# Performance work log

Measured on AMD Instinct MI355X. Metric: run time of the kernel, lower is better.

The kernel has to match this reference:

```python
import jax, jax.numpy as jnp
import numpy as np

WS = (7, 7, 7)
SS = (3, 3, 3)
SEQ = WS[0] * WS[1] * WS[2]  # 343
EPS = 1e-5


def layer_norm(x, w, b):
    mu = jnp.mean(x, axis=-1, keepdims=True)
    var = jnp.mean((x - mu) ** 2, axis=-1, keepdims=True)
    return (x - mu) * jax.lax.rsqrt(var + EPS) * w + b


def window_partition(x, ws):
    b, d, h, w, c = x.shape
    x = x.reshape(b, d // ws[0], ws[0], h // ws[1], ws[1], w // ws[2], ws[2], c)
    return x.transpose(0, 1, 3, 5, 2, 4, 6, 7).reshape(-1, ws[0] * ws[1] * ws[2], c)


def window_reverse(win, ws, dims):
    b, dp, hp, wp = dims
    x = win.reshape(b, dp // ws[0], hp // ws[1], wp // ws[2], ws[0], ws[1], ws[2], -1)
    return x.transpose(0, 1, 4, 2, 5, 3, 6, 7).reshape(b, dp, hp, wp, -1)


def _rel_pos_index():
    coords = np.stack(np.meshgrid(np.arange(WS[0]), np.arange(WS[1]), np.arange(WS[2]), indexing='ij'))
    cf = coords.reshape(3, -1)
    rel = (cf[:, :, None] - cf[:, None, :]).transpose(1, 2, 0)  # (s, s, 3)
    rel[..., 0] += WS[0] - 1
    rel[..., 1] += WS[1] - 1
    rel[..., 2] += WS[2] - 1
    idx = rel[..., 0] * (2 * WS[1] - 1) * (2 * WS[2] - 1) + rel[..., 1] * (2 * WS[2] - 1) + rel[..., 2]
    return idx.astype(np.int32)


def _swin_mask(dp, hp, wp):
    img = np.zeros((1, dp, hp, wp, 1), np.float32)
    cnt = 0
    sl = lambda ws, ss: (slice(0, -ws), slice(-ws, -ss), slice(-ss, None))
    for ds in sl(WS[0], SS[0]):
        for hs in sl(WS[1], SS[1]):
            for wsl in sl(WS[2], SS[2]):
                img[:, ds, hs, wsl, :] = cnt
                cnt += 1
    mw = np.asarray(window_partition(jnp.asarray(img), WS)).squeeze(-1)  # (nW, s)
    am = mw[:, None, :] - mw[:, :, None]
    return np.where(am != 0, np.float32(-100.0), np.float32(0.0))


def setup_inputs() -> dict:
    key = jax.random.key(0)
    ks = jax.random.split(key, 12)
    B, D, H, W, C = 1, 28, 56, 28, 192
    NH, DH = 6, 32
    FFI = 4 * C
    L = 2
    s = 0.02
    inp = {
        'x': jax.random.normal(ks[0], (B, D, H, W, C), jnp.float32),
        'mask_matrix': jnp.asarray(_swin_mask(D, H, W)),
        'clinical': jax.random.normal(ks[1], (B, 8), jnp.float32),
        'ln1_w': jnp.ones((L, C)), 'ln1_b': jnp.zeros((L, C)),
        'qkv_w': jax.random.normal(ks[2], (L, C, 3 * C)) * s, 'qkv_b': jnp.zeros((L, 3 * C)),
        'out_w': jax.random.normal(ks[3], (L, C, C)) * s, 'out_b': jnp.zeros((L, C)),
        'ln2_w': jnp.ones((L, C)), 'ln2_b': jnp.zeros((L, C)),
        'ff1_w': jax.random.normal(ks[4], (L, C, 2 * FFI)) * s, 'ff1_b': jnp.zeros((L, 2 * FFI)),
        'ff2_w': jax.random.normal(ks[5], (L, FFI, C)) * s, 'ff2_b': jnp.zeros((L, C)),
        'rpb': jax.random.normal(ks[6], (L, (2 * WS[0] - 1) * (2 * WS[1] - 1) * (2 * WS[2] - 1), NH)) * s,
        'lnf_w': jnp.ones((C,)), 'lnf_b': jnp.zeros((C,)),
        'rel_index': jnp.asarray(_rel_pos_index()),
    }
    return inp


def reference(x, mask_matrix, clinical, ln1_w, ln1_b, qkv_w, qkv_b, out_w, out_b,
              ln2_w, ln2_b, ff1_w, ff1_b, ff2_w, ff2_b, rpb, lnf_w, lnf_b, rel_index):
    b, d, h, w, c = x.shape
    nh = rpb.shape[-1]
    dh = c // nh
    # pad to window multiples (no-op for chosen shapes, kept for fidelity)
    pd = (WS[0] - d % WS[0]) % WS[0]
    ph = (WS[1] - h % WS[1]) % WS[1]
    pw = (WS[2] - w % WS[2]) % WS[2]
    xp = jnp.pad(x, ((0, 0), (0, pd), (0, ph), (0, pw), (0, 0)))
    dp, hp, wp = d + pd, h + ph, w + pw
    # cyclic shift
    xs = jnp.roll(xp, shift=(-SS[0], -SS[1], -SS[2]), axis=(1, 2, 3))
    xw = window_partition(xs, WS)  # (nW*b, s, c)
    # mask: values {0,-100} -> allowed bool (True = attend), per source math
    allowed = jnp.logical_not((mask_matrix * (-1.0 / 100.0)).astype(bool))[:, None, :, :]
    scale = 1.0 / jnp.sqrt(jnp.asarray(dh, xw.dtype))
    for l in range(2):
        hdn = layer_norm(xw, ln1_w[l], ln1_b[l])
        qkv = hdn @ qkv_w[l] + qkv_b[l]
        q, k, v = jnp.split(qkv, 3, axis=-1)
        q = q.reshape(-1, SEQ, nh, dh).transpose(0, 2, 1, 3)
        k = k.reshape(-1, SEQ, nh, dh).transpose(0, 2, 1, 3)
        v = v.reshape(-1, SEQ, nh, dh).transpose(0, 2, 1, 3)
        scores = jnp.einsum('whqd,whkd->whqk', q, k) * scale
        bias = rpb[l][rel_index].transpose(2, 0, 1)  # (nh, s, s)
        scores = scores + bias[None]
        scores = jnp.where(allowed, scores, jnp.asarray(-1e9, scores.dtype))
        attn = jax.nn.softmax(scores, axis=-1)
        o = jnp.einsum('whqk,whkd->whqd', attn, v).transpose(0, 2, 1, 3).reshape(-1, SEQ, c)
        xw = xw + (o @ out_w[l] + out_b[l])
        f = layer_norm(xw, ln2_w[l], ln2_b[l]) @ ff1_w[l] + ff1_b[l]
        u, g = jnp.split(f, 2, axis=-1)  # GLU feed-forward
        xw = xw + ((u * jax.nn.gelu(g)) @ ff2_w[l] + ff2_b[l])
    xw = layer_norm(xw, lnf_w, lnf_b)
    aw = xw.reshape(-1, WS[0], WS[1], WS[2], c)
    xs = window_reverse(aw, WS, (b, dp, hp, wp))
    xo = jnp.roll(xs, shift=(SS[0], SS[1], SS[2]), axis=(1, 2, 3))
    return xo[:, :d, :h, :w, :]
```

## Files before the change

### kernel.cpp

```cpp
#include <hip/hip_runtime.h>
#include <hip/hip_fp16.h>
#include <math.h>

#define SEQ 343
#define CCH 192
#define NWIN 128
#define NHEAD 6
#define TOK (NWIN * SEQ)

typedef __bf16 bf16x8 __attribute__((ext_vector_type(8)));
typedef float f32x4 __attribute__((ext_vector_type(4)));
typedef float f32x16 __attribute__((ext_vector_type(16)));
typedef unsigned short ushort8 __attribute__((ext_vector_type(8)));
typedef _Float16 half8 __attribute__((ext_vector_type(8)));
typedef _Float16 hv2 __attribute__((ext_vector_type(2)));

__device__ __forceinline__ unsigned short f2bf(float f) {
    unsigned u = __float_as_uint(f);
    u += 0x7FFF + ((u >> 16) & 1);
    return (unsigned short)(u >> 16);
}

__device__ __forceinline__ float gelu_tanh(float x) {
    const float k0 = 0.7978845608028654f;
    const float k1 = 0.044715f;
    float y = k0 * (x + k1 * x * x * x);
    float t = 1.0f - 2.0f / (__expf(2.0f * y) + 1.0f);
    return 0.5f * x * (1.0f + t);
}

__device__ __forceinline__ void gld16(void* l, const void* g) {
    __builtin_amdgcn_global_load_lds((const __attribute__((address_space(1))) unsigned int*)g,
                                     (__attribute__((address_space(3))) unsigned int*)l, 16, 0, 0);
}

__device__ __forceinline__ hv2 pkrtz(float a, float b) {
    return __builtin_bit_cast(hv2, __builtin_amdgcn_cvt_pkrtz(a, b));
}
__device__ __forceinline__ hv2 u2h2(unsigned u) { return __builtin_bit_cast(hv2, u); }
__device__ __forceinline__ unsigned h22u(hv2 h) { return __builtin_bit_cast(unsigned, h); }

__global__ __launch_bounds__(256) void k_shift_part(const float* __restrict__ x,
                                                    float* __restrict__ xw) {
    int idx = blockIdx.x * 256 + threadIdx.x;
    if (idx >= TOK * 48) return;
    int c4 = idx % 48;
    int tok = idx / 48;
    int t = tok % SEQ;
    int wn = tok / SEQ;
    int tw = t % 7, th = (t / 7) % 7, td = t / 49;
    int ww = wn & 3, wh = (wn >> 2) & 7, wd = wn >> 5;
    int sd = (wd * 7 + td + 3) % 28;
    int sh = (wh * 7 + th + 3) % 56;
    int sw = (ww * 7 + tw + 3) % 28;
    const float4* src = (const float4*)(x + (size_t)((sd * 56 + sh) * 28 + sw) * CCH);
    ((float4*)xw)[idx] = src[c4];
}

__global__ __launch_bounds__(256) void k_ln_bf(const float* __restrict__ in,
                                               const float* __restrict__ w,
                                               const float* __restrict__ b,
                                               unsigned short* __restrict__ out, int rows) {
    int row = blockIdx.x * 4 + (threadIdx.x >> 6);
    int lane = threadIdx.x & 63;
    if (row >= rows) return;
    const float* p = in + (size_t)row * CCH;
    float v0 = p[lane], v1 = p[lane + 64], v2 = p[lane + 128];
    float s = v0 + v1 + v2;
#pragma unroll
    for (int off = 32; off > 0; off >>= 1) s += __shfl_xor(s, off);
    float mu = s * (1.0f / 192.0f);
    float d0 = v0 - mu, d1 = v1 - mu, d2 = v2 - mu;
    float vv = d0 * d0 + d1 * d1 + d2 * d2;
#pragma unroll
    for (int off = 32; off > 0; off >>= 1) vv += __shfl_xor(vv, off);
    float rs = rsqrtf(vv * (1.0f / 192.0f) + 1e-5f);
    unsigned short* q = out + (size_t)row * CCH;
    q[lane] = f2bf(d0 * rs * w[lane] + b[lane]);
    q[lane + 64] = f2bf(d1 * rs * w[lane + 64] + b[lane + 64]);
    q[lane + 128] = f2bf(d2 * rs * w[lane + 128] + b[lane + 128]);
}

__global__ __launch_bounds__(256) void k_ln_out(const float* __restrict__ xw,
                                                const float* __restrict__ w,
                                                const float* __restrict__ b,
                                                float* __restrict__ out) {
    int row = blockIdx.x * 4 + (threadIdx.x >> 6);
    int lane = threadIdx.x & 63;
    if (row >= TOK) return;
    int d = row / 1568;
    int hh = (row / 28) % 56;
    int wv = row % 28;
    int sd = (d + 25) % 28, sh = (hh + 53) % 56, sw = (wv + 25) % 28;
    int wn = (sd / 7) * 32 + (sh / 7) * 4 + (sw / 7);
    int t = (sd % 7) * 49 + (sh % 7) * 7 + (sw % 7);
    const float* p = xw + ((size_t)wn * SEQ + t) * CCH;
    float v0 = p[lane], v1 = p[lane + 64], v2 = p[lane + 128];
    float s = v0 + v1 + v2;
#pragma unroll
    for (int off = 32; off > 0; off >>= 1) s += __shfl_xor(s, off);
    float mu = s * (1.0f / 192.0f);
    float d0 = v0 - mu, d1 = v1 - mu, d2 = v2 - mu;
    float vv = d0 * d0 + d1 * d1 + d2 * d2;
#pragma unroll
    for (int off = 32; off > 0; off >>= 1) vv += __shfl_xor(vv, off);
    float rs = rsqrtf(vv * (1.0f / 192.0f) + 1e-5f);
    float* q = out + (size_t)row * CCH;
    q[lane] = d0 * rs * w[lane] + b[lane];
    q[lane + 64] = d1 * rs * w[lane + 64] + b[lane + 64];
    q[lane + 128] = d2 * rs * w[lane + 128] + b[lane + 128];
}

__global__ __launch_bounds__(256) void k_wprep(const float* __restrict__ qkv_w,
                                               const float* __restrict__ out_w,
                                               const float* __restrict__ ff1_w,
                                               const float* __restrict__ ff2_w,
                                               unsigned short* __restrict__ wt) {
    int idx = blockIdx.x * 256 + threadIdx.x;
    if (idx >= 1179648) return;
    int l = idx / 589824;
    int r = idx - l * 589824;
    const float* src;
    int Kd, Nd, off;
    if (r < 110592)      { src = qkv_w + (size_t)l * 110592; Kd = 192; Nd = 576;  off = r; }
    else if (r < 147456) { src = out_w + (size_t)l * 36864;  Kd = 192; Nd = 192;  off = r - 110592; }
    else if (r < 442368) { src = ff1_w + (size_t)l * 294912; Kd = 192; Nd = 1536; off = r - 147456; }
    else                 { src = ff2_w + (size_t)l * 147456; Kd = 768; Nd = 192;  off = r - 442368; }
    int n = off / Kd, k = off - n * Kd;
    wt[idx] = f2bf(src[(size_t)k * Nd + n]);
}

__global__ void k_cbgen3(const float* __restrict__ mask, const float* __restrict__ rpb,
                         uint2* __restrict__ cb4) {
    int q = threadIdx.x;
    int k4 = blockIdx.x;
    int h = blockIdx.y;
    int cl = blockIdx.z;
    int wn = ((cl & 4) ? 96 : 0) + ((cl & 2) ? 28 : 0) + ((cl & 1) ? 3 : 0);
    const float LOG2E = 1.4426950408889634f;
    int qd = q / 49, qh = (q / 7) % 7, qw = q % 7;
    unsigned v[4];
#pragma unroll
    for (int t = 0; t < 4; ++t) {
        int k = 4 * k4 + t;
        float val = -14000.0f;
        if (k < SEQ && q < SEQ) {
            float mk = mask[((size_t)wn * SEQ + k) * SEQ + q];
            if (mk == 0.0f) {
                int kd = k / 49, kh = (k / 7) % 7, kw = k % 7;
                int rel = (qd - kd + 6) * 169 + (qh - kh + 6) * 13 + (qw - kw + 6);
                val = rpb[(size_t)rel * NHEAD + h] * LOG2E;
            }
        }
        v[t] = __half_as_ushort(__float2half_rn(val));
    }
    uint2 pk = {v[0] | (v[1] << 16), v[2] | (v[3] << 16)};
    cb4[((size_t)(cl * NHEAD + h) * 88 + k4) * 352 + q] = pk;
}

template <int MODE>
__global__ __launch_bounds__(256) void k_gemm32(const unsigned short* __restrict__ A,
                                                const unsigned short* __restrict__ Wt,
                                                const float* __restrict__ bias,
                                                float* __restrict__ outF,
                                                unsigned short* __restrict__ outB,
                                                _Float16* __restrict__ outH,
                                                _Float16* __restrict__ outV,
                                                int N, int K) {
    constexpr int BN = (MODE == 0) ? 192 : 64;
    constexpr int NF = (MODE == 0) ? 3 : 1;
    constexpr int WNC = NF * 32;
    constexpr int BROWS = (MODE == 0) ? 192 : ((MODE == 2) ? 128 : 64);
    constexpr int BCH = (BROWS * 128) / 4096;
    __shared__ char AsB[16384];
    __shared__ char BsB[BROWS * 128];
    const int tid = threadIdx.x;
    const int n0 = blockIdx.x * BN;
    const size_t m0 = (size_t)blockIdx.y * 128;
    const int lane = tid & 63, wid = tid >> 6;
    const int wm = wid >> 1, wn = wid & 1;
    const int ln31 = lane & 31, hi16 = (lane >> 5) * 16;
    const int xorv = (ln31 & 7) << 4;
    const size_t ldb = (size_t)K * 2;

    f32x16 acc[2][NF];
    f32x16 accG[2];
#pragma unroll
    for (int mi = 0; mi < 2; ++mi) {
#pragma unroll
        for (int nj = 0; nj < NF; ++nj) acc[mi][nj] = (f32x16)(0.f);
        accG[mi] = (f32x16)(0.f);
    }

    for (int kb = 0; kb < K; kb += 64) {
#pragma unroll
        for (int i = 0; i < 4; ++i) {
            int s = i * 4096 + tid * 16;
            int r = s >> 7;
            int cb = (s & 127) ^ ((r & 7) << 4);
            gld16(AsB + s, (const char*)A + (m0 + r) * ldb + (size_t)kb * 2 + cb);
        }
#pragma unroll
        for (int i = 0; i < BCH; ++i) {
            int s = i * 4096 + tid * 16;
            int r = s >> 7;
            int cb = (s & 127) ^ ((r & 7) << 4);
            int grow = n0 + r + ((MODE == 2 && r >= 64) ? 704 : 0);
            gld16(BsB + s, (const char*)Wt + (size_t)grow * ldb + (size_t)kb * 2 + cb);
        }
        __syncthreads();
#pragma unroll
        for (int ks = 0; ks < 4; ++ks) {
            const int ccb = (ks * 32 + hi16) ^ xorv;
            bf16x8 a0 = *(const bf16x8*)(AsB + (wm * 64 + ln31) * 128 + ccb);
            bf16x8 a1 = *(const bf16x8*)(AsB + (wm * 64 + 32 + ln31) * 128 + ccb);
            if (MODE == 2) {
                bf16x8 bu = *(const bf16x8*)(BsB + (wn * 32 + ln31) * 128 + ccb);
                bf16x8 bg = *(const bf16x8*)(BsB + (64 + wn * 32 + ln31) * 128 + ccb);
                acc[0][0] = __builtin_amdgcn_mfma_f32_32x32x16_bf16(a0, bu, acc[0][0], 0, 0, 0);
                acc[1][0] = __builtin_amdgcn_mfma_f32_32x32x16_bf16(a1, bu, acc[1][0], 0, 0, 0);
                accG[0] = __builtin_amdgcn_mfma_f32_32x32x16_bf16(a0, bg, accG[0], 0, 0, 0);
                accG[1] = __builtin_amdgcn_mfma_f32_32x32x16_bf16(a1, bg, accG[1], 0, 0, 0);
            } else {
#pragma unroll
                for (int nj = 0; nj < NF; ++nj) {
                    bf16x8 b = *(const bf16x8*)(BsB + (wn * WNC + nj * 32 + ln31) * 128 + ccb);
                    acc[0][nj] = __builtin_amdgcn_mfma_f32_32x32x16_bf16(a0, b, acc[0][nj], 0, 0, 0);
                    acc[1][nj] = __builtin_amdgcn_mfma_f32_32x32x16_bf16(a1, b, acc[1][nj], 0, 0, 0);
                }
            }
        }
        __syncthreads();
    }

    const float S2LOG = 0.17677669529663687f * 1.4426950408889634f;
    const int rbase = (int)m0 + wm * 64 + ((lane >> 5) << 2);
    const int cbase = n0 + wn * WNC + ln31;
#pragma unroll
    for (int mi = 0; mi < 2; ++mi) {
#pragma unroll
        for (int nj = 0; nj < NF; ++nj) {
            const int gc = cbase + nj * 32;
            const float bb = bias[gc];
            const float bgv = (MODE == 2) ? bias[768 + gc] : 0.f;
#pragma unroll
            for (int reg = 0; reg < 16; ++reg) {
                const int row = rbase + mi * 32 + (reg & 3) + ((reg >> 2) << 3);
                float v = acc[mi][nj][reg] + bb;
                if (MODE == 1) {
                    outF[(size_t)row * N + gc] += v;
                } else if (MODE == 0) {
                    if (n0 < 384) {
                        outH[(size_t)row * 384 + gc] = (_Float16)(n0 == 0 ? v * S2LOG : v);
                    } else {
                        int d = gc - 384, hh = d >> 5, dd = d & 31;
                        int wnn = row / 343, qq = row - wnn * 343;
                        outV[(((size_t)wnn * NHEAD + hh) * 32 + dd) * 344 + qq] = (_Float16)v;
                    }
                } else {
                    float g = accG[mi][reg] + bgv;
                    outB[(size_t)row * 768 + gc] = f2bf(v * gelu_tanh(g));
                }
            }
        }
    }
}

__global__ __launch_bounds__(256) void k_attn4(const _Float16* __restrict__ qk,
                                               const _Float16* __restrict__ vt,
                                               const uint2* __restrict__ cb4,
                                               unsigned short* __restrict__ o) {
    __shared__ _Float16 Ks[352 * 32];
    __shared__ _Float16 Vt[32 * 352];
    const int h = blockIdx.x;
    const int wn = blockIdx.y;
    const int tid = threadIdx.x;
    const _Float16* kbase = qk + (size_t)wn * SEQ * 384 + 192 + h * 32;
    for (int j = tid; j < 1408; j += 256) {
        int s = j >> 2, c = j & 3;
        int slot = c ^ ((s >> 2) & 3);
        *(half8*)&Ks[s * 32 + slot * 8] = *(const half8*)&kbase[(size_t)s * 384 + c * 8];
    }
    const _Float16* vbase = vt + ((size_t)wn * NHEAD + h) * 32 * 344;
    for (int j = tid; j < 1408; j += 256) {
        int d = j / 44, ch = j % 44;
        int slot = ch ^ ((d >> 2) & 3);
        *(half8*)&Vt[d * 352 + slot * 8] = *(const half8*)&vbase[(size_t)d * 344 + ch * 8];
    }
    __syncthreads();
    const int wid = tid >> 6, lane = tid & 63;
    const int qloc = lane & 15, g = lane >> 4;
    const int xq = (qloc >> 2) & 3;
    const int slotK = (g ^ xq) * 8;
    const int iA = (qloc | ((g & 1) << 5)) * 4;
    const int iB = iA + 64;
    const bool ghi = g >= 2;
    int cls = (((wn >> 5) == 3) ? 4 : 0) | ((((wn >> 2) & 7) == 7) ? 2 : 0) | (((wn & 3) == 3) ? 1 : 0);
    const uint2* cbb = cb4 + (size_t)(cls * NHEAD + h) * 88 * 352;
    for (int qt = wid; qt < 22; qt += 4) {
        const int q0 = qt * 16;
        const int qrow = q0 + qloc;
        half8 qf = *(const half8*)&qk[((size_t)wn * SEQ + qrow) * 384 + h * 32 + g * 8];
        unsigned spk[22][2];
        hv2 mpk = {(_Float16)(-60000.0f), (_Float16)(-60000.0f)};
        __builtin_amdgcn_s_setprio(1);
#pragma unroll
        for (int kt = 0; kt < 22; ++kt) {
            half8 kf = *(const half8*)&Ks[(kt * 16 + qloc) * 32 + slotK];
            f32x4 st = __builtin_amdgcn_mfma_f32_16x16x32_f16(kf, qf, (f32x4){0.f, 0.f, 0.f, 0.f}, 0, 0, 0);
            uint2 cv = cbb[(size_t)(kt * 4 + g) * 352 + qrow];
            hv2 s01 = pkrtz(st[0], st[1]) + u2h2(cv.x);
            hv2 s23 = pkrtz(st[2], st[3]) + u2h2(cv.y);
            mpk = __builtin_elementwise_max(mpk, __builtin_elementwise_max(s01, s23));
            spk[kt][0] = h22u(s01);
            spk[kt][1] = h22u(s23);
        }
        __builtin_amdgcn_s_setprio(0);
        float mf = fmaxf((float)mpk[0], (float)mpk[1]);
        mf = fmaxf(mf, __shfl_xor(mf, 16));
        mf = fmaxf(mf, __shfl_xor(mf, 32));
        float l = 0.f;
#pragma unroll
        for (int kt = 0; kt < 22; ++kt) {
            hv2 s01 = u2h2(spk[kt][0]);
            hv2 s23 = u2h2(spk[kt][1]);
            float e0 = exp2f((float)s01[0] - mf), e1 = exp2f((float)s01[1] - mf);
            float e2 = exp2f((float)s23[0] - mf), e3 = exp2f((float)s23[1] - mf);
            l += (e0 + e1) + (e2 + e3);
            spk[kt][0] = h22u(pkrtz(e0, e1));
            spk[kt][1] = h22u(pkrtz(e2, e3));
        }
        l += __shfl_xor(l, 16);
        l += __shfl_xor(l, 32);
        f32x4 acc0 = {0.f, 0.f, 0.f, 0.f}, acc1 = {0.f, 0.f, 0.f, 0.f};
        __builtin_amdgcn_s_setprio(1);
#pragma unroll
        for (int ch = 0; ch < 11; ++ch) {
            unsigned a0 = __builtin_amdgcn_ds_bpermute(iA, spk[2 * ch][0]);
            unsigned a1 = __builtin_amdgcn_ds_bpermute(iA, spk[2 * ch][1]);
            unsigned a2 = __builtin_amdgcn_ds_bpermute(iB, spk[2 * ch][0]);
            unsigned a3 = __builtin_amdgcn_ds_bpermute(iB, spk[2 * ch][1]);
            unsigned b0 = __builtin_amdgcn_ds_bpermute(iA, spk[2 * ch + 1][0]);
            unsigned b1 = __builtin_amdgcn_ds_bpermute(iA, spk[2 * ch + 1][1]);
            unsigned b2 = __builtin_amdgcn_ds_bpermute(iB, spk[2 * ch + 1][0]);
            unsigned b3 = __builtin_amdgcn_ds_bpermute(iB, spk[2 * ch + 1][1]);
            uint4 pfu = {ghi ? b0 : a0, ghi ? b1 : a1, ghi ? b2 : a2, ghi ? b3 : a3};
            half8 pf = __builtin_bit_cast(half8, pfu);
            const int slotV = ((ch * 4 + g) ^ xq) * 8;
            half8 v0 = *(const half8*)&Vt[qloc * 352 + slotV];
            half8 v1 = *(const half8*)&Vt[(qloc + 16) * 352 + slotV];
            acc0 = __builtin_amdgcn_mfma_f32_16x16x32_f16(v0, pf, acc0, 0, 0, 0);
            acc1 = __builtin_amdgcn_mfma_f32_16x16x32_f16(v1, pf, acc1, 0, 0, 0);
        }
        __builtin_amdgcn_s_setprio(0);
        if (qrow < SEQ) {
            float inv = 1.0f / l;
            unsigned short* orow = o + ((size_t)wn * SEQ + qrow) * CCH + h * 32;
            ushort4 w0 = {f2bf(acc0[0] * inv), f2bf(acc0[1] * inv),
                          f2bf(acc0[2] * inv), f2bf(acc0[3] * inv)};
            ushort4 w1 = {f2bf(acc1[0] * inv), f2bf(acc1[1] * inv),
                          f2bf(acc1[2] * inv), f2bf(acc1[3] * inv)};
            *(ushort4*)&orow[g * 4] = w0;
            *(ushort4*)&orow[16 + g * 4] = w1;
        }
    }
}

extern "C" void kernel_launch(void* const* d_in, const int* in_sizes, int n_in,
                              void* d_out, int out_size, void* d_ws, size_t ws_size,
                              hipStream_t stream) {
    const float* x     = (const float*)d_in[0];
    const float* mask  = (const float*)d_in[1];
    const float* ln1_w = (const float*)d_in[3];
    const float* ln1_b = (const float*)d_in[4];
    const float* qkv_w = (const float*)d_in[5];
    const float* qkv_b = (const float*)d_in[6];
    const float* out_w = (const float*)d_in[7];
    const float* out_b = (const float*)d_in[8];
    const float* ln2_w = (const float*)d_in[9];
    const float* ln2_b = (const float*)d_in[10];
    const float* ff1_w = (const float*)d_in[11];
    const float* ff1_b = (const float*)d_in[12];
    const float* ff2_w = (const float*)d_in[13];
    const float* ff2_b = (const float*)d_in[14];
    const float* rpb   = (const float*)d_in[15];
    const float* lnf_w = (const float*)d_in[16];
    const float* lnf_b = (const float*)d_in[17];

    char* wsp = (char*)d_ws;
    float* xw = (float*)wsp;                          wsp += (size_t)TOK * 192 * 4;
    unsigned short* hdnb = (unsigned short*)wsp;      wsp += (size_t)TOK * 192 * 2;
    _Float16* qkh = (_Float16*)wsp;                   wsp += (size_t)TOK * 384 * 2;
    _Float16* vth = (_Float16*)wsp;                   wsp += (size_t)NWIN * NHEAD * 32 * 344 * 2;
    unsigned short* glub = (unsigned short*)wsp;      wsp += (size_t)TOK * 768 * 2;
    unsigned short* wt = (unsigned short*)wsp;        wsp += (size_t)1179648 * 2;
    uint2* cb4 = (uint2*)wsp;
    float* out = (float*)d_out;

    k_shift_part<<<8232, 256, 0, stream>>>(x, xw);
    k_wprep<<<4608, 256, 0, stream>>>(qkv_w, out_w, ff1_w, ff2_w, wt);
    for (int l = 0; l < 2; ++l) {
        unsigned short* wbase = wt + (size_t)l * 589824;
        k_cbgen3<<<dim3(88, NHEAD, 8), 352, 0, stream>>>(mask, rpb + (size_t)l * 2197 * NHEAD, cb4);
        k_ln_bf<<<10976, 256, 0, stream>>>(xw, ln1_w + l * 192, ln1_b + l * 192, hdnb, TOK);
        k_gemm32<0><<<dim3(3, 343), 256, 0, stream>>>(hdnb, wbase, qkv_b + l * 576,
                                                      nullptr, nullptr, qkh, vth, 576, 192);
        k_attn4<<<dim3(NHEAD, NWIN), 256, 0, stream>>>(qkh, vth, cb4, hdnb);
        k_gemm32<1><<<dim3(3, 343), 256, 0, stream>>>(hdnb, wbase + 110592, out_b + l * 192,
                                                      xw, nullptr, nullptr, nullptr, 192, 192);
        k_ln_bf<<<10976, 256, 0, stream>>>(xw, ln2_w + l * 192, ln2_b + l * 192, hdnb, TOK);
        k_gemm32<2><<<dim3(12, 343), 256, 0, stream>>>(hdnb, wbase + 147456, ff1_b + l * 1536,
                                                       nullptr, glub, nullptr, nullptr, 768, 192);
        k_gemm32<1><<<dim3(3, 343), 256, 0, stream>>>(glub, wbase + 442368, ff2_b + l * 192,
                                                      xw, nullptr, nullptr, nullptr, 192, 768);
    }
    k_ln_out<<<10976, 256, 0, stream>>>(xw, lnf_w, lnf_b, out);
}
```

Baseline: 694.6 us.

## Fuse softmax exponentiation into PV loop and stage P through shared memory

The attention kernel now computes the exponentials inside the P·V loop instead of in a separate pass. Each wave writes its exponentiated probabilities to a small per-wave LDS buffer and reads them back in MFMA operand layout, replacing the eight ds_bpermute shuffles per chunk. The LDS swizzles for K and V are also changed, and out-of-range K, V and Q rows are now zero-filled rather than read past the sequence end. The aim is less register-shuffle traffic and better overlap of exp work with MFMA. The cost is extra LDS writes and reads per chunk, and a possible intra-wave ordering hazard on Pb.

```diff
diff --git a/kernel.cpp b/kernel.cpp
--- a/kernel.cpp
+++ b/kernel.cpp
@@ -13,6 +13,7 @@
 typedef float f32x16 __attribute__((ext_vector_type(16)));
 typedef unsigned short ushort8 __attribute__((ext_vector_type(8)));
 typedef _Float16 half8 __attribute__((ext_vector_type(8)));
+typedef _Float16 half4 __attribute__((ext_vector_type(4)));
 typedef _Float16 hv2 __attribute__((ext_vector_type(2)));
 
 __device__ __forceinline__ unsigned short f2bf(float f) {
@@ -266,41 +267,52 @@
     }
 }
 
-__global__ __launch_bounds__(256) void k_attn4(const _Float16* __restrict__ qk,
+__global__ __launch_bounds__(256) void k_attn5(const _Float16* __restrict__ qk,
                                                const _Float16* __restrict__ vt,
                                                const uint2* __restrict__ cb4,
                                                unsigned short* __restrict__ o) {
     __shared__ _Float16 Ks[352 * 32];
     __shared__ _Float16 Vt[32 * 352];
+    __shared__ _Float16 Pb[4 * 16 * 32];
     const int h = blockIdx.x;
     const int wn = blockIdx.y;
     const int tid = threadIdx.x;
     const _Float16* kbase = qk + (size_t)wn * SEQ * 384 + 192 + h * 32;
     for (int j = tid; j < 1408; j += 256) {
         int s = j >> 2, c = j & 3;
-        int slot = c ^ ((s >> 2) & 3);
-        *(half8*)&Ks[s * 32 + slot * 8] = *(const half8*)&kbase[(size_t)s * 384 + c * 8];
+        int slot = c ^ (s & 3);
+        half8 v = {};
+        if (s < SEQ) v = *(const half8*)&kbase[(size_t)s * 384 + c * 8];
+        *(half8*)&Ks[s * 32 + slot * 8] = v;
     }
     const _Float16* vbase = vt + ((size_t)wn * NHEAD + h) * 32 * 344;
     for (int j = tid; j < 1408; j += 256) {
-        int d = j / 44, ch = j % 44;
-        int slot = ch ^ ((d >> 2) & 3);
-        *(half8*)&Vt[d * 352 + slot * 8] = *(const half8*)&vbase[(size_t)d * 344 + ch * 8];
+        int d = j / 44, c = j % 44;
+        int slot = c ^ (d & 3);
+        int cb8 = c * 8;
+        half8 v = {};
+        if (cb8 + 7 <= 342) {
+            v = *(const half8*)&vbase[(size_t)d * 344 + cb8];
+        } else if (cb8 <= 342) {
+#pragma unroll
+            for (int i = 0; i < 8; ++i) v[i] = (cb8 + i <= 342) ? vbase[(size_t)d * 344 + cb8 + i] : (_Float16)0.f;
+        }
+        *(half8*)&Vt[d * 352 + slot * 8] = v;
     }
     __syncthreads();
     const int wid = tid >> 6, lane = tid & 63;
     const int qloc = lane & 15, g = lane >> 4;
-    const int xq = (qloc >> 2) & 3;
-    const int slotK = (g ^ xq) * 8;
-    const int iA = (qloc | ((g & 1) << 5)) * 4;
-    const int iB = iA + 64;
-    const bool ghi = g >= 2;
+    const int x3 = qloc & 3;
+    const int x6 = qloc & 6;
+    const int slotK = (g ^ x3) * 8;
+    const int pb = (wid * 16 + qloc) * 32;
     int cls = (((wn >> 5) == 3) ? 4 : 0) | ((((wn >> 2) & 7) == 7) ? 2 : 0) | (((wn & 3) == 3) ? 1 : 0);
     const uint2* cbb = cb4 + (size_t)(cls * NHEAD + h) * 88 * 352;
     for (int qt = wid; qt < 22; qt += 4) {
         const int q0 = qt * 16;
         const int qrow = q0 + qloc;
-        half8 qf = *(const half8*)&qk[((size_t)wn * SEQ + qrow) * 384 + h * 32 + g * 8];
+        half8 qf = {};
+        if (qrow < SEQ) qf = *(const half8*)&qk[((size_t)wn * SEQ + qrow) * 384 + h * 32 + g * 8];
         unsigned spk[22][2];
         hv2 mpk = {(_Float16)(-60000.0f), (_Float16)(-60000.0f)};
         __builtin_amdgcn_s_setprio(1);
@@ -320,39 +332,29 @@
         mf = fmaxf(mf, __shfl_xor(mf, 16));
         mf = fmaxf(mf, __shfl_xor(mf, 32));
         float l = 0.f;
-#pragma unroll
-        for (int kt = 0; kt < 22; ++kt) {
-            hv2 s01 = u2h2(spk[kt][0]);
-            hv2 s23 = u2h2(spk[kt][1]);
-            float e0 = exp2f((float)s01[0] - mf), e1 = exp2f((float)s01[1] - mf);
-            float e2 = exp2f((float)s23[0] - mf), e3 = exp2f((float)s23[1] - mf);
-            l += (e0 + e1) + (e2 + e3);
-            spk[kt][0] = h22u(pkrtz(e0, e1));
-            spk[kt][1] = h22u(pkrtz(e2, e3));
-        }
-        l += __shfl_xor(l, 16);
-        l += __shfl_xor(l, 32);
         f32x4 acc0 = {0.f, 0.f, 0.f, 0.f}, acc1 = {0.f, 0.f, 0.f, 0.f};
-        __builtin_amdgcn_s_setprio(1);
 #pragma unroll
         for (int ch = 0; ch < 11; ++ch) {
-            unsigned a0 = __builtin_amdgcn_ds_bpermute(iA, spk[2 * ch][0]);
-            unsigned a1 = __builtin_amdgcn_ds_bpermute(iA, spk[2 * ch][1]);
-            unsigned a2 = __builtin_amdgcn_ds_bpermute(iB, spk[2 * ch][0]);
-            unsigned a3 = __builtin_amdgcn_ds_bpermute(iB, spk[2 * ch][1]);
-            unsigned b0 = __builtin_amdgcn_ds_bpermute(iA, spk[2 * ch + 1][0]);
-            unsigned b1 = __builtin_amdgcn_ds_bpermute(iA, spk[2 * ch + 1][1]);
-            unsigned b2 = __builtin_amdgcn_ds_bpermute(iB, spk[2 * ch + 1][0]);
-            unsigned b3 = __builtin_amdgcn_ds_bpermute(iB, spk[2 * ch + 1][1]);
-            uint4 pfu = {ghi ? b0 : a0, ghi ? b1 : a1, ghi ? b2 : a2, ghi ? b3 : a3};
-            half8 pf = __builtin_bit_cast(half8, pfu);
-            const int slotV = ((ch * 4 + g) ^ xq) * 8;
+            hv2 a0 = u2h2(spk[2 * ch][0]), a1 = u2h2(spk[2 * ch][1]);
+            hv2 b0 = u2h2(spk[2 * ch + 1][0]), b1 = u2h2(spk[2 * ch + 1][1]);
+            float e0 = exp2f((float)a0[0] - mf), e1 = exp2f((float)a0[1] - mf);
+            float e2 = exp2f((float)a1[0] - mf), e3 = exp2f((float)a1[1] - mf);
+            float e4 = exp2f((float)b0[0] - mf), e5 = exp2f((float)b0[1] - mf);
+            float e6 = exp2f((float)b1[0] - mf), e7 = exp2f((float)b1[1] - mf);
+            l += ((e0 + e1) + (e2 + e3)) + ((e4 + e5) + (e6 + e7));
+            uint2 wlo = {h22u(pkrtz(e0, e1)), h22u(pkrtz(e2, e3))};
+            uint2 whi = {h22u(pkrtz(e4, e5)), h22u(pkrtz(e6, e7))};
+            *(uint2*)&Pb[pb + ((g ^ x6) << 2)] = wlo;
+            *(uint2*)&Pb[pb + (((4 + g) ^ x6) << 2)] = whi;
+            half8 pf = *(const half8*)&Pb[pb + (((2 * g) ^ x6) << 2)];
+            const int slotV = ((ch * 4 + g) ^ x3) * 8;
             half8 v0 = *(const half8*)&Vt[qloc * 352 + slotV];
             half8 v1 = *(const half8*)&Vt[(qloc + 16) * 352 + slotV];
             acc0 = __builtin_amdgcn_mfma_f32_16x16x32_f16(v0, pf, acc0, 0, 0, 0);
             acc1 = __builtin_amdgcn_mfma_f32_16x16x32_f16(v1, pf, acc1, 0, 0, 0);
         }
-        __builtin_amdgcn_s_setprio(0);
+        l += __shfl_xor(l, 16);
+        l += __shfl_xor(l, 32);
         if (qrow < SEQ) {
             float inv = 1.0f / l;
             unsigned short* orow = o + ((size_t)wn * SEQ + qrow) * CCH + h * 32;
@@ -405,7 +407,7 @@
         k_ln_bf<<<10976, 256, 0, stream>>>(xw, ln1_w + l * 192, ln1_b + l * 192, hdnb, TOK);
         k_gemm32<0><<<dim3(3, 343), 256, 0, stream>>>(hdnb, wbase, qkv_b + l * 576,
                                                       nullptr, nullptr, qkh, vth, 576, 192);
-        k_attn4<<<dim3(NHEAD, NWIN), 256, 0, stream>>>(qkh, vth, cb4, hdnb);
+        k_attn5<<<dim3(NHEAD, NWIN), 256, 0, stream>>>(qkh, vth, cb4, hdnb);
         k_gemm32<1><<<dim3(3, 343), 256, 0, stream>>>(hdnb, wbase + 110592, out_b + l * 192,
                                                       xw, nullptr, nullptr, nullptr, 192, 192);
         k_ln_bf<<<10976, 256, 0, stream>>>(xw, ln2_w + l * 192, ln2_b + l * 192, hdnb, TOK);
```

After: 620.5 us. 1.12x faster.
